# Kernel optimization log

Measured on AMD Instinct MI355X. Metric: run time of the kernel, lower is better.

Reference implementation:

```python
import jax, jax.numpy as jnp
import numpy as np


def _gru_dirs(x, h, w_ih, w_hh, b_ih, b_hh):
    # One GRU step for both directions at once (seq_len==1 per original loop).
    # x: [N, in], h: [2, N, H]; w_ih: [2, 3H, in], w_hh: [2, 3H, H], biases [2, 3H]
    gi = jnp.einsum('ni,dgi->dng', x, w_ih) + b_ih[:, None, :]
    gh = jnp.einsum('dnh,dgh->dng', h, w_hh) + b_hh[:, None, :]
    H = h.shape[-1]
    ir, iz, inn = gi[..., :H], gi[..., H:2 * H], gi[..., 2 * H:]
    hr, hz, hn = gh[..., :H], gh[..., H:2 * H], gh[..., 2 * H:]
    r = jax.nn.sigmoid(ir + hr)
    z = jax.nn.sigmoid(iz + hz)
    n = jnp.tanh(inn + r * hn)
    return (1.0 - z) * n + z * h


def setup_inputs() -> dict:
    key = jax.random.key(0)
    ks = jax.random.split(key, 6)
    V, E, H, NL = 32000, 1024, 512, 2  # vocab, input_size, hidden_size, num_layers
    N, L = 32, 512
    s = 0.05
    x = jax.random.randint(ks[0], (N, L), 0, V)
    emb = jax.random.normal(ks[1], (V, E), dtype=jnp.float32) * s
    w_ih = jax.random.normal(ks[2], (NL, 2, 3 * H, E), dtype=jnp.float32) * s
    w_hh = jax.random.normal(ks[3], (NL, 2, 3 * H, H), dtype=jnp.float32) * s
    b_ih = jax.random.normal(ks[4], (NL, 2, 3 * H), dtype=jnp.float32) * s
    b_hh = jax.random.normal(ks[5], (NL, 2, 3 * H), dtype=jnp.float32) * s
    return {"x": x, "emb": emb, "w_ih": w_ih, "w_hh": w_hh, "b_ih": b_ih, "b_hh": b_hh}


def reference(x, emb, w_ih, w_hh, b_ih, b_hh):
    # Because the torch code calls the bidirectional GRU one timestep at a time
    # with a carried hidden, BOTH directions scan left-to-right over the sequence.
    N, L = x.shape
    num_layers = w_ih.shape[0]
    H = w_hh.shape[-1]
    h0 = jnp.zeros((num_layers, 2, N, H), dtype=emb.dtype)

    def step(h, xt):
        layer_in = emb[xt]  # [N, E] embedding lookup for this timestep
        new_h = []
        for l in range(num_layers):  # fixed small layer loop
            hl = _gru_dirs(layer_in, h[l], w_ih[l], w_hh[l], b_ih[l], b_hh[l])
            new_h.append(hl)
            layer_in = jnp.concatenate([hl[0], hl[1]], axis=-1)  # [N, 2H]
        hs = jnp.stack(new_h)  # [num_layers, 2, N, H]
        return hs, (layer_in, hs)

    _, (outs, hiddens) = jax.lax.scan(step, h0, x.T)  # scan over L timesteps
    outputs = jnp.transpose(outs, (1, 0, 2))  # [N, L, 2H]
    hiddens = hiddens.reshape(L, num_layers * 2, N, H)  # [L, 2*num_layers, N, H]
    return outputs, hiddens
```

## Files before the change

### kernel.cpp

```cpp
#include <hip/hip_runtime.h>
#include <hip/hip_bf16.h>

using u16 = unsigned short;
using u32 = unsigned int;
using bf16x8 = __attribute__((ext_vector_type(8))) __bf16;
using f32x4  = __attribute__((ext_vector_type(4))) float;
using u32x2  = __attribute__((ext_vector_type(2))) u32;
using u32x4  = __attribute__((ext_vector_type(4))) u32;

#define GLP(p) ((const __attribute__((address_space(1))) void*)(p))
#define LDSP(p) ((__attribute__((address_space(3))) void*)(p))

__device__ __forceinline__ float bf2f(u16 u) {
    union { float f; u32 i; } v; v.i = ((u32)u) << 16; return v.f;
}
__device__ __forceinline__ u16 f2bf(float f) {
    union { float f; u32 i; } v; v.f = f;
    u32 r = v.i + 0x7FFFu + ((v.i >> 16) & 1u);
    return (u16)(r >> 16);
}

__device__ __forceinline__ u32 ld_sc01_u32(const u32* p) {
    u32 v;
    asm volatile("global_load_dword %0, %1, off sc0 sc1\n\ts_waitcnt vmcnt(0)"
                 : "=v"(v) : "v"(p) : "memory");
    return v;
}
__device__ __forceinline__ void st_sc01_u32(u32* p, u32 v) {
    asm volatile("global_store_dword %0, %1, off sc0 sc1" :: "v"(p), "v"(v) : "memory");
}
__device__ __forceinline__ void st_sc01_u32x2(u32* p, u32x2 v) {
    asm volatile("global_store_dwordx2 %0, %1, off sc0 sc1" :: "v"(p), "v"(v) : "memory");
}
__device__ __forceinline__ void st_sc01_u16(u16* p, u16 v) {
    asm volatile("global_store_short %0, %1, off sc0 sc1" :: "v"(p), "v"(v) : "memory");
}

__device__ __forceinline__ float sigm(float x) {
    return __builtin_amdgcn_rcpf(1.f + __expf(-x));
}
__device__ __forceinline__ float tanh_fast(float x) {
    float e = __expf(-2.f * x);
    return (1.f - e) * __builtin_amdgcn_rcpf(1.f + e);
}

__global__ void k_gather(const int* __restrict__ x, const float* __restrict__ emb,
                         u16* __restrict__ X0) {
    int gid = blockIdx.x * blockDim.x + threadIdx.x;
    if (gid >= 16384 * 256) return;
    int e4 = gid << 2;
    int m = e4 >> 10, k = e4 & 1023;
    int t = m >> 5, n = m & 31;
    int tok = x[n * 512 + t];
    float4 v = *reinterpret_cast<const float4*>(emb + ((size_t)tok << 10) + k);
    ushort4 o;
    o.x = f2bf(v.x); o.y = f2bf(v.y); o.z = f2bf(v.z); o.w = f2bf(v.w);
    *reinterpret_cast<ushort4*>(X0 + (size_t)e4) = o;
}

__global__ void k_f32bf16(const float* __restrict__ s, u16* __restrict__ d, int n4) {
    int gid = blockIdx.x * blockDim.x + threadIdx.x;
    if (gid >= n4) return;
    float4 v = reinterpret_cast<const float4*>(s)[gid];
    ushort4 o;
    o.x = f2bf(v.x); o.y = f2bf(v.y); o.z = f2bf(v.z); o.w = f2bf(v.w);
    reinterpret_cast<ushort4*>(d)[gid] = o;
}

template<int LAYER>
__device__ __forceinline__ void gru_body(char* smem, int d, int wg,
    const u16* __restrict__ Gi, const u16* __restrict__ Whh_l,
    const float* __restrict__ bhh_l, u32* __restrict__ hbuf,
    u16* __restrict__ X1, float* __restrict__ hid, float* __restrict__ outp,
    u32* __restrict__ xflags, const u32* __restrict__ gdone)
{
    char* hS          = smem;
    float (*ghs)[196] = (float(*)[196])(smem + 32768);
    u16 (*gis)[208]   = (u16(*)[208])(smem + 57856);
    float* bhh_s      = (float*)(smem + 71168);
    const int tid = threadIdx.x;
    const int lane = tid & 63, w = tid >> 6;
    const int j0 = wg * 64;
    const int g = w >> 2;
    const int lr = lane & 15, lk = lane >> 4;

    if (tid < 192) {
        int g2 = tid >> 6, jj = tid & 63;
        bhh_s[tid] = bhh_l[d * 1536 + g2 * 512 + j0 + jj];
    }
    bf16x8 wf[16];
    {
        const int joff = (w & 3) * 16;
        const u16* wr = Whh_l + (size_t)(d * 1536 + g * 512 + j0 + joff + lr) * 512 + lk * 8;
        #pragma unroll
        for (int kt = 0; kt < 16; ++kt)
            wf[kt] = *reinterpret_cast<const bf16x8*>(wr + kt * 32);
    }
    __syncthreads();

    const int colu = w * 64 + (lane & 7) * 8;
    const int rb = lane >> 3;
    const int cb = colu * 2;
    const int ci0 = (tid - 512) * 3;

    float hpv[4] = {0.f, 0.f, 0.f, 0.f};
    u32 g_seen = 0;

    for (int t = 0; t < 512; ++t) {
        if (w < 8) {
            const u32* hb = hbuf + ((size_t)d * 2 + ((t + 1) & 1)) * 16384;
            const u32 expt = (u32)t << 16;
            u32x4 va[4][2];
            bool fresh[4] = {false, false, false, false};
            long long T0 = __builtin_amdgcn_s_memrealtime();
            for (;;) {
                #pragma unroll
                for (int c = 0; c < 4; ++c) {
                    if (!fresh[c]) {
                        const u32* p = hb + (size_t)(rb + c * 8) * 512 + colu;
                        asm volatile("global_load_dwordx4 %0, %1, off sc0 sc1"
                                     : "=v"(va[c][0]) : "v"(p));
                        asm volatile("global_load_dwordx4 %0, %1, off sc0 sc1"
                                     : "=v"(va[c][1]) : "v"(p + 4));
                    }
                }
                asm volatile("s_waitcnt vmcnt(0)" ::: "memory");
                bool all4 = true;
                #pragma unroll
                for (int c = 0; c < 4; ++c) {
                    if (!fresh[c]) {
                        u32 xv = 0;
                        #pragma unroll
                        for (int i = 0; i < 4; ++i) {
                            xv |= (va[c][0][i] ^ expt);
                            xv |= (va[c][1][i] ^ expt);
                        }
                        fresh[c] = ((xv & 0xFFFF0000u) == 0);
                    }
                    all4 = all4 && fresh[c];
                }
                if (__all(all4)) break;
                if (__builtin_amdgcn_s_memrealtime() - T0 > 2000000) break;
            }
            #pragma unroll
            for (int c = 0; c < 4; ++c) {
                int row = rb + c * 8;
                u32x4 pk;
                pk[0] = (va[c][0][0] & 0xFFFFu) | (va[c][0][1] << 16);
                pk[1] = (va[c][0][2] & 0xFFFFu) | (va[c][0][3] << 16);
                pk[2] = (va[c][1][0] & 0xFFFFu) | (va[c][1][1] << 16);
                pk[3] = (va[c][1][2] & 0xFFFFu) | (va[c][1][3] << 16);
                *reinterpret_cast<u32x4*>(hS + row * 1024 + (cb ^ ((row & 15) << 4))) = pk;
            }
        } else {
            u32 yneed = (u32)(t >> 2);
            if (g_seen <= yneed) {
                const u32* gp = gdone + yneed;
                long long T0 = __builtin_amdgcn_s_memrealtime();
                while (ld_sc01_u32(gp) == 0) {
                    __builtin_amdgcn_s_sleep(1);
                    if (__builtin_amdgcn_s_memrealtime() - T0 > 2000000) break;
                }
                g_seen = yneed + 1;
            }
            u32x4 gq[3];
            int nbs[3], gcs[3];
            #pragma unroll
            for (int i = 0; i < 3; ++i) {
                int ci = ci0 + i;
                nbs[i] = ci / 24; gcs[i] = ci % 24;
                const u16* gp = Gi + (size_t)(t * 32 + nbs[i]) * 3072 + d * 1536
                              + (gcs[i] >> 3) * 512 + j0 + (gcs[i] & 7) * 8;
                asm volatile("global_load_dwordx4 %0, %1, off sc0 sc1"
                             : "=v"(gq[i]) : "v"(gp));
            }
            asm volatile("s_waitcnt vmcnt(0)" ::: "memory");
            #pragma unroll
            for (int i = 0; i < 3; ++i)
                *reinterpret_cast<u32x4*>(&gis[nbs[i]][gcs[i] * 8]) = gq[i];
        }
        __syncthreads();

        f32x4 acc0 = {0.f, 0.f, 0.f, 0.f}, acc1 = acc0;
        #pragma unroll
        for (int kt = 0; kt < 16; ++kt) {
            int boff = (lk * 16 + kt * 64) ^ (lr << 4);
            bf16x8 a0 = *reinterpret_cast<const bf16x8*>(hS + lr * 1024 + boff);
            bf16x8 a1 = *reinterpret_cast<const bf16x8*>(hS + (16 + lr) * 1024 + boff);
            acc0 = __builtin_amdgcn_mfma_f32_16x16x32_bf16(a0, wf[kt], acc0, 0, 0, 0);
            acc1 = __builtin_amdgcn_mfma_f32_16x16x32_bf16(a1, wf[kt], acc1, 0, 0, 0);
        }
        int colg = w * 16 + lr;
        float bv = bhh_s[colg];
        #pragma unroll
        for (int q = 0; q < 4; ++q) {
            ghs[lk * 4 + q][colg]      = acc0[q] + bv;
            ghs[16 + lk * 4 + q][colg] = acc1[q] + bv;
        }
        __syncthreads();

        u32* hbw = hbuf + ((size_t)d * 2 + (t & 1)) * 16384;
        const u32 tagn = (u32)(t + 1) << 16;
        #pragma unroll
        for (int rep = 0; rep < 2; ++rep) {
            int e2 = (rep == 0) ? tid : tid + 256;
            if (rep == 0 || tid >= 512) {
                int jp = (e2 & 31) * 2, nb = e2 >> 5;
                int rr = rep * 2;
                float r0 = sigm(bf2f(gis[nb][jp])          + ghs[nb][jp]);
                float r1 = sigm(bf2f(gis[nb][jp + 1])      + ghs[nb][jp + 1]);
                float z0 = sigm(bf2f(gis[nb][64 + jp])     + ghs[nb][64 + jp]);
                float z1 = sigm(bf2f(gis[nb][64 + jp + 1]) + ghs[nb][64 + jp + 1]);
                float n0 = tanh_fast(bf2f(gis[nb][128 + jp])     + r0 * ghs[nb][128 + jp]);
                float n1 = tanh_fast(bf2f(gis[nb][128 + jp + 1]) + r1 * ghs[nb][128 + jp + 1]);
                float hv0 = (1.f - z0) * n0 + z0 * hpv[rr];
                float hv1 = (1.f - z1) * n1 + z1 * hpv[rr + 1];
                hpv[rr] = hv0; hpv[rr + 1] = hv1;
                u16 b0 = f2bf(hv0), b1 = f2bf(hv1);
                u32x2 pp = { (u32)b0 | tagn, (u32)b1 | tagn };
                st_sc01_u32x2(hbw + (size_t)nb * 512 + j0 + jp, pp);
                float2 hf; hf.x = hv0; hf.y = hv1;
                *reinterpret_cast<float2*>(hid + ((size_t)(t * 4 + LAYER * 2 + d) * 32 + nb) * 512
                                           + j0 + jp) = hf;
                if (LAYER == 0) {
                    st_sc01_u32((u32*)(X1 + (size_t)(t * 32 + nb) * 1024 + (size_t)d * 512 + j0 + jp),
                                (u32)b0 | ((u32)b1 << 16));
                } else {
                    *reinterpret_cast<float2*>(outp + ((size_t)nb * 512 + t) * 1024
                                               + (size_t)d * 512 + j0 + jp) = hf;
                }
            }
        }
        if (LAYER == 0 && (t & 3) == 3) {
            asm volatile("s_waitcnt vmcnt(0)" ::: "memory");
            __syncthreads();
            if (tid == 17)
                st_sc01_u32(xflags + (d * 8 + wg) * 32, (u32)(t + 1));
        } else {
            __builtin_amdgcn_sched_barrier(0);
            __builtin_amdgcn_s_barrier();
            __builtin_amdgcn_sched_barrier(0);
        }
    }
}

__device__ __forceinline__ void chaser_body(char* smem, int cw,
    const u16* __restrict__ A, const u16* __restrict__ B,
    const float* __restrict__ bias, u16* __restrict__ Gi,
    const u32* __restrict__ xflags, u32* __restrict__ cnt, u32* __restrict__ done)
{
    u16* As = (u16*)smem;
    u16* Bs = (u16*)(smem + 16384);
    const int tid = threadIdx.x;
    const int lane = tid & 63, wid = tid >> 6;
    const int wm = wid & 1, wn = wid >> 1;
    const int lr = lane & 15, lk = lane >> 4;

    for (int T = cw; T < 4096; T += 48) {
        const int y = T >> 5, x = T & 31;
        if (xflags && tid < 16) {
            const u32* fp = xflags + tid * 32;
            u32 target = 4u * (u32)y + 4u;
            long long T0 = __builtin_amdgcn_s_memrealtime();
            while (ld_sc01_u32(fp) < target) {
                __builtin_amdgcn_s_sleep(4);
                if (__builtin_amdgcn_s_memrealtime() - T0 > 2000000) break;
            }
        }
        __syncthreads();

        f32x4 zero = {0.f, 0.f, 0.f, 0.f};
        f32x4 acc[4][2];
        #pragma unroll
        for (int i = 0; i < 4; ++i) { acc[i][0] = zero; acc[i][1] = zero; }

        for (int k0 = 0; k0 < 1024; k0 += 64) {
            #pragma unroll
            for (int r = 0; r < 5; ++r) {
                int c = wid * 5 + r;
                if (c < 16) {
                    int o = c * 1024 + lane * 16;
                    int row = o >> 7, kb = o & 127;
                    int kbs = kb ^ ((row & 7) << 4);
                    const char* s = (const char*)A + ((size_t)(y * 128 + row) * 1024 + k0) * 2 + kbs;
                    __builtin_amdgcn_global_load_lds(GLP(s), LDSP((char*)As + c * 1024), 16, 0, 0);
                } else if (c < 28) {
                    int c2 = c - 16;
                    int o = c2 * 1024 + lane * 16;
                    int row = o >> 7, kb = o & 127;
                    int kbs = kb ^ ((row & 7) << 4);
                    const char* s = (const char*)B + ((size_t)(x * 96 + row) * 1024 + k0) * 2 + kbs;
                    __builtin_amdgcn_global_load_lds(GLP(s), LDSP((char*)Bs + c2 * 1024), 16, 0, 0);
                }
            }
            __syncthreads();
            if (wid < 6) {
                #pragma unroll
                for (int kk = 0; kk < 2; ++kk) {
                    bf16x8 af[4], bfr[2];
                    int kb = kk * 64 + lk * 16;
                    #pragma unroll
                    for (int i = 0; i < 4; ++i) {
                        int rowA = wm * 64 + i * 16 + lr;
                        af[i] = *reinterpret_cast<const bf16x8*>((const char*)As + rowA * 128 + (kb ^ ((rowA & 7) << 4)));
                    }
                    #pragma unroll
                    for (int j = 0; j < 2; ++j) {
                        int rowB = wn * 32 + j * 16 + lr;
                        bfr[j] = *reinterpret_cast<const bf16x8*>((const char*)Bs + rowB * 128 + (kb ^ ((rowB & 7) << 4)));
                    }
                    #pragma unroll
                    for (int i = 0; i < 4; ++i)
                        #pragma unroll
                        for (int j = 0; j < 2; ++j)
                            acc[i][j] = __builtin_amdgcn_mfma_f32_16x16x32_bf16(af[i], bfr[j], acc[i][j], 0, 0, 0);
                }
            }
            __syncthreads();
        }
        if (wid < 6) {
            #pragma unroll
            for (int j = 0; j < 2; ++j) {
                int col = x * 96 + wn * 32 + j * 16 + lr;
                float bv = bias[col];
                #pragma unroll
                for (int i = 0; i < 4; ++i) {
                    int rowb = y * 128 + wm * 64 + i * 16 + lk * 4;
                    #pragma unroll
                    for (int q = 0; q < 4; ++q)
                        st_sc01_u16(Gi + (size_t)(rowb + q) * 3072 + col, f2bf(acc[i][j][q] + bv));
                }
            }
        }
        asm volatile("s_waitcnt vmcnt(0)" ::: "memory");
        __syncthreads();
        if (tid == 0) {
            u32 old = __hip_atomic_fetch_add(&cnt[y], 1u, __ATOMIC_RELAXED,
                                             __HIP_MEMORY_SCOPE_AGENT);
            if (old == 31u)
                st_sc01_u32((u32*)&done[y], 1u);
        }
    }
}

__global__ __launch_bounds__(768, 3) void k_fused(
    u16* __restrict__ Gi,
    const u16* __restrict__ X0, const u16* __restrict__ Wih,
    const float* __restrict__ b_ih,
    const u16* __restrict__ Whh, const float* __restrict__ bhh,
    u32* __restrict__ hbuf0, u32* __restrict__ hbuf1,
    u16* __restrict__ X1,
    float* __restrict__ hid, float* __restrict__ outp,
    u32* __restrict__ xflags,
    u32* __restrict__ g0cnt, u32* __restrict__ g0done,
    u32* __restrict__ g1cnt, u32* __restrict__ g1done)
{
    __shared__ __align__(16) char smem[71936];
    int bid = blockIdx.x;
    if (bid < 16) {
        gru_body<0>(smem, bid >> 3, bid & 7, Gi, Whh, bhh, hbuf0,
                    X1, hid, outp, xflags, g0done);
    } else if (bid < 64) {
        chaser_body(smem, bid - 16, X0, Wih, b_ih, Gi, nullptr, g0cnt, g0done);
    } else if (bid < 112) {
        chaser_body(smem, bid - 64, X1, Wih + (size_t)3072 * 1024, b_ih + 3072,
                    Gi, xflags, g1cnt, g1done);
    } else {
        int b = bid - 112;
        gru_body<1>(smem, b >> 3, b & 7, Gi, Whh + (size_t)3072 * 512, bhh + 3072,
                    hbuf1, nullptr, hid, outp, nullptr, g1done);
    }
}

extern "C" void kernel_launch(void* const* d_in, const int* in_sizes, int n_in,
                              void* d_out, int out_size, void* d_ws, size_t ws_size,
                              hipStream_t stream) {
    const int*   x    = (const int*)d_in[0];
    const float* emb  = (const float*)d_in[1];
    const float* w_ih = (const float*)d_in[2];
    const float* w_hh = (const float*)d_in[3];
    const float* b_ih = (const float*)d_in[4];
    const float* b_hh = (const float*)d_in[5];
    float* outp = (float*)d_out;
    float* hid  = outp + (size_t)32 * 512 * 1024;

    char* ws = (char*)d_ws;
    u16* X0     = (u16*)(ws);
    u16* X1     = (u16*)(ws + 33554432);
    u16* Wih    = (u16*)(ws + 67108864);
    u16* Whh    = (u16*)(ws + 79691776);
    u16* Gi     = (u16*)(ws + 85983232);
    u32* hbuf0  = (u32*)(ws + 186646528);
    u32* hbuf1  = (u32*)(ws + 186908672);
    u32* xflags = (u32*)(ws + 187170816);
    u32* g0cnt  = (u32*)(ws + 187172864);
    u32* g0done = (u32*)(ws + 187173376);
    u32* g1cnt  = (u32*)(ws + 187173888);
    u32* g1done = (u32*)(ws + 187174400);

    k_gather<<<16384, 256, 0, stream>>>(x, emb, X0);
    k_f32bf16<<<(1572864 + 255) / 256, 256, 0, stream>>>(w_ih, Wih, 1572864);
    k_f32bf16<<<( 786432 + 255) / 256, 256, 0, stream>>>(w_hh, Whh, 786432);

    (void)hipMemsetAsync(hbuf0, 0, 528384, stream);

    k_fused<<<128, 768, 0, stream>>>(Gi, X0, Wih, b_ih, Whh, b_hh,
                                     hbuf0, hbuf1, X1, hid, outp,
                                     xflags, g0cnt, g0done, g1cnt, g1done);
}
```

Before: 2.370 ms.

## Add per-workgroup step flags and defer output stores to spare waves

Each GRU workgroup now publishes a per-step flag, and consumer waves poll the flags of their producer workgroups before polling the tagged hidden buffer. The flag poll uses sleep and a timeout fallback that self-publishes. The hidden, X1 and output stores are moved out of the gate loop: bf16 values are staged in LDS, and the otherwise idle waves 8-11 write them as wider vector stores after a barrier, taking them off the critical path. The change also raises wave priority, lowers launch bounds occupancy from 3 to 2, and grows the LDS and flag workspace. The risks are extra polling latency per step and the loss of fp32 precision in the hid and output writes, which are now rebuilt from bf16.

```diff
diff --git a/kernel.cpp b/kernel.cpp
--- a/kernel.cpp
+++ b/kernel.cpp
@@ -34,6 +34,9 @@
 }
 __device__ __forceinline__ void st_sc01_u16(u16* p, u16 v) {
     asm volatile("global_store_short %0, %1, off sc0 sc1" :: "v"(p), "v"(v) : "memory");
+}
+__device__ __forceinline__ void st_sc01_u32x4(u16* p, u32x4 v) {
+    asm volatile("global_store_dwordx4 %0, %1, off sc0 sc1" :: "v"(p), "v"(v) : "memory");
 }
 
 __device__ __forceinline__ float sigm(float x) {
@@ -72,17 +75,20 @@
     const u16* __restrict__ Gi, const u16* __restrict__ Whh_l,
     const float* __restrict__ bhh_l, u32* __restrict__ hbuf,
     u16* __restrict__ X1, float* __restrict__ hid, float* __restrict__ outp,
-    u32* __restrict__ xflags, const u32* __restrict__ gdone)
+    u32* __restrict__ flags, u32* __restrict__ xflags, const u32* __restrict__ gdone)
 {
     char* hS          = smem;
     float (*ghs)[196] = (float(*)[196])(smem + 32768);
     u16 (*gis)[208]   = (u16(*)[208])(smem + 57856);
     float* bhh_s      = (float*)(smem + 71168);
+    u16* hvS          = (u16*)(smem + 71936);
     const int tid = threadIdx.x;
     const int lane = tid & 63, w = tid >> 6;
     const int j0 = wg * 64;
     const int g = w >> 2;
     const int lr = lane & 15, lk = lane >> 4;
+
+    __builtin_amdgcn_s_setprio(1);
 
     if (tid < 192) {
         int g2 = tid >> 6, jj = tid & 63;
@@ -98,6 +104,9 @@
     }
     __syncthreads();
 
+    u32* myflag = flags + (d * 8 + wg) * 32;
+    const u32* wflag = flags + (d * 8 + (w & 7)) * 32;
+
     const int colu = w * 64 + (lane & 7) * 8;
     const int rb = lane >> 3;
     const int cb = colu * 2;
@@ -108,6 +117,18 @@
 
     for (int t = 0; t < 512; ++t) {
         if (w < 8) {
+            if (t > 0) {
+                long long tt0 = __builtin_amdgcn_s_memrealtime();
+                while (ld_sc01_u32(wflag) < (u32)t) {
+                    __builtin_amdgcn_s_sleep(1);
+                    if (__builtin_amdgcn_s_memrealtime() - tt0 > 2000) {
+                        if (lane == 0)
+                            __hip_atomic_store(myflag, (u32)t, __ATOMIC_RELEASE,
+                                               __HIP_MEMORY_SCOPE_AGENT);
+                        tt0 = __builtin_amdgcn_s_memrealtime();
+                    }
+                }
+            }
             const u32* hb = hbuf + ((size_t)d * 2 + ((t + 1) & 1)) * 16384;
             const u32 expt = (u32)t << 16;
             u32x4 va[4][2];
@@ -203,8 +224,8 @@
         const u32 tagn = (u32)(t + 1) << 16;
         #pragma unroll
         for (int rep = 0; rep < 2; ++rep) {
-            int e2 = (rep == 0) ? tid : tid + 256;
-            if (rep == 0 || tid >= 512) {
+            int e2 = tid + rep * 768;
+            if (e2 < 1024) {
                 int jp = (e2 & 31) * 2, nb = e2 >> 5;
                 int rr = rep * 2;
                 float r0 = sigm(bf2f(gis[nb][jp])          + ghs[nb][jp]);
@@ -219,16 +240,32 @@
                 u16 b0 = f2bf(hv0), b1 = f2bf(hv1);
                 u32x2 pp = { (u32)b0 | tagn, (u32)b1 | tagn };
                 st_sc01_u32x2(hbw + (size_t)nb * 512 + j0 + jp, pp);
-                float2 hf; hf.x = hv0; hf.y = hv1;
-                *reinterpret_cast<float2*>(hid + ((size_t)(t * 4 + LAYER * 2 + d) * 32 + nb) * 512
-                                           + j0 + jp) = hf;
-                if (LAYER == 0) {
-                    st_sc01_u32((u32*)(X1 + (size_t)(t * 32 + nb) * 1024 + (size_t)d * 512 + j0 + jp),
-                                (u32)b0 | ((u32)b1 << 16));
-                } else {
-                    *reinterpret_cast<float2*>(outp + ((size_t)nb * 512 + t) * 1024
-                                               + (size_t)d * 512 + j0 + jp) = hf;
-                }
+                *reinterpret_cast<u32*>(hvS + nb * 64 + jp) = (u32)b0 | ((u32)b1 << 16);
+            }
+        }
+        asm volatile("s_waitcnt lgkmcnt(0)" ::: "memory");
+        __builtin_amdgcn_sched_barrier(0);
+        __builtin_amdgcn_s_barrier();
+        __builtin_amdgcn_sched_barrier(0);
+        if (tid == 528)
+            st_sc01_u32(myflag, (u32)(t + 1));
+
+        if (tid >= 512) {
+            int q = tid - 512, nb = q >> 3, j8 = (q & 7) * 8;
+            union { u32x4 v; u16 s[8]; } h8;
+            h8.v = *reinterpret_cast<const u32x4*>(hvS + nb * 64 + j8);
+            float f0 = bf2f(h8.s[0]), f1 = bf2f(h8.s[1]), f2 = bf2f(h8.s[2]), f3 = bf2f(h8.s[3]);
+            float f4 = bf2f(h8.s[4]), f5 = bf2f(h8.s[5]), f6 = bf2f(h8.s[6]), f7 = bf2f(h8.s[7]);
+            float* hp = hid + ((size_t)(t * 4 + LAYER * 2 + d) * 32 + nb) * 512 + j0 + j8;
+            *reinterpret_cast<float4*>(hp)     = make_float4(f0, f1, f2, f3);
+            *reinterpret_cast<float4*>(hp + 4) = make_float4(f4, f5, f6, f7);
+            if (LAYER == 0) {
+                u16* xp = X1 + (size_t)(t * 32 + nb) * 1024 + (size_t)d * 512 + j0 + j8;
+                st_sc01_u32x4(xp, h8.v);
+            } else {
+                float* op = outp + ((size_t)nb * 512 + t) * 1024 + (size_t)d * 512 + j0 + j8;
+                *reinterpret_cast<float4*>(op)     = make_float4(f0, f1, f2, f3);
+                *reinterpret_cast<float4*>(op + 4) = make_float4(f4, f5, f6, f7);
             }
         }
         if (LAYER == 0 && (t & 3) == 3) {
@@ -236,10 +273,6 @@
             __syncthreads();
             if (tid == 17)
                 st_sc01_u32(xflags + (d * 8 + wg) * 32, (u32)(t + 1));
-        } else {
-            __builtin_amdgcn_sched_barrier(0);
-            __builtin_amdgcn_s_barrier();
-            __builtin_amdgcn_sched_barrier(0);
         }
     }
 }
@@ -343,7 +376,7 @@
     }
 }
 
-__global__ __launch_bounds__(768, 3) void k_fused(
+__global__ __launch_bounds__(768, 2) void k_fused(
     u16* __restrict__ Gi,
     const u16* __restrict__ X0, const u16* __restrict__ Wih,
     const float* __restrict__ b_ih,
@@ -351,15 +384,16 @@
     u32* __restrict__ hbuf0, u32* __restrict__ hbuf1,
     u16* __restrict__ X1,
     float* __restrict__ hid, float* __restrict__ outp,
+    u32* __restrict__ flags0, u32* __restrict__ flags1,
     u32* __restrict__ xflags,
     u32* __restrict__ g0cnt, u32* __restrict__ g0done,
     u32* __restrict__ g1cnt, u32* __restrict__ g1done)
 {
-    __shared__ __align__(16) char smem[71936];
+    __shared__ __align__(16) char smem[76032];
     int bid = blockIdx.x;
     if (bid < 16) {
         gru_body<0>(smem, bid >> 3, bid & 7, Gi, Whh, bhh, hbuf0,
-                    X1, hid, outp, xflags, g0done);
+                    X1, hid, outp, flags0, xflags, g0done);
     } else if (bid < 64) {
         chaser_body(smem, bid - 16, X0, Wih, b_ih, Gi, nullptr, g0cnt, g0done);
     } else if (bid < 112) {
@@ -368,7 +402,7 @@
     } else {
         int b = bid - 112;
         gru_body<1>(smem, b >> 3, b & 7, Gi, Whh + (size_t)3072 * 512, bhh + 3072,
-                    hbuf1, nullptr, hid, outp, nullptr, g1done);
+                    hbuf1, nullptr, hid, outp, flags1, nullptr, g1done);
     }
 }
 
@@ -392,19 +426,22 @@
     u16* Gi     = (u16*)(ws + 85983232);
     u32* hbuf0  = (u32*)(ws + 186646528);
     u32* hbuf1  = (u32*)(ws + 186908672);
-    u32* xflags = (u32*)(ws + 187170816);
-    u32* g0cnt  = (u32*)(ws + 187172864);
-    u32* g0done = (u32*)(ws + 187173376);
-    u32* g1cnt  = (u32*)(ws + 187173888);
-    u32* g1done = (u32*)(ws + 187174400);
+    u32* flags0 = (u32*)(ws + 187170816);
+    u32* flags1 = (u32*)(ws + 187172864);
+    u32* xflags = (u32*)(ws + 187174912);
+    u32* g0cnt  = (u32*)(ws + 187176960);
+    u32* g0done = (u32*)(ws + 187177472);
+    u32* g1cnt  = (u32*)(ws + 187177984);
+    u32* g1done = (u32*)(ws + 187178496);
 
     k_gather<<<16384, 256, 0, stream>>>(x, emb, X0);
     k_f32bf16<<<(1572864 + 255) / 256, 256, 0, stream>>>(w_ih, Wih, 1572864);
     k_f32bf16<<<( 786432 + 255) / 256, 256, 0, stream>>>(w_hh, Whh, 786432);
 
-    (void)hipMemsetAsync(hbuf0, 0, 528384, stream);
+    (void)hipMemsetAsync(hbuf0, 0, 532480, stream);
 
     k_fused<<<128, 768, 0, stream>>>(Gi, X0, Wih, b_ih, Whh, b_hh,
                                      hbuf0, hbuf1, X1, hid, outp,
-                                     xflags, g0cnt, g0done, g1cnt, g1done);
-}
+                                     flags0, flags1, xflags,
+                                     g0cnt, g0done, g1cnt, g1done);
+}
```

New measurement: 2.442 ms. 1.03x slower.
